# Performance work log

Measured on AMD Instinct MI355X. Metric: run time of the kernel, lower is better.

The kernel has to match this reference:

```python
import jax, jax.numpy as jnp
import numpy as np

N_NODES = 40000
N_EDGES = 640000
N_GRAPHS = 64
F_IN = 32       # fourier_order*4
D_EMB = 256     # int(0.5*512)
D_HID = 512     # int(0.5*1024)
D_FC = 1024     # int(0.5*2048)
N_CLS = 10


def setup_inputs() -> dict:
    key = jax.random.key(0)
    ks = iter(jax.random.split(key, 40))
    rn = lambda shape, s=0.05: jax.random.normal(next(ks), shape, jnp.float32) * s
    inp = {
        'x': jax.random.normal(next(ks), (N_NODES, F_IN), jnp.float32),
        'edge_index': jax.random.randint(next(ks), (2, N_EDGES), 0, N_NODES, jnp.int32),
        'edge_attr': jax.random.uniform(next(ks), (N_EDGES, 1), jnp.float32),
        'batch': jnp.sort(jax.random.randint(next(ks), (N_NODES,), 0, N_GRAPHS, jnp.int32)),
        # embedding MLP
        'emb_w1': rn((F_IN, D_EMB)), 'emb_b1': jnp.zeros((D_EMB,), jnp.float32),
        'emb_w2': rn((D_EMB, D_EMB)), 'emb_b2': jnp.zeros((D_EMB,), jnp.float32),
        # edge_proj MLP
        'ep_w1': rn((1, 64)), 'ep_b1': jnp.zeros((64,), jnp.float32),
        'ep_w2': rn((64, 1)), 'ep_b2': jnp.zeros((1,), jnp.float32),
        # GCNConv weights (x @ W + b, PyG convention)
        'w_c1': rn((D_EMB, D_HID)), 'b_c1': jnp.zeros((D_HID,), jnp.float32),
        'w_c2': rn((D_HID, D_HID)), 'b_c2': jnp.zeros((D_HID,), jnp.float32),
        'w_c3': rn((D_HID, D_HID)), 'b_c3': jnp.zeros((D_HID,), jnp.float32),
        'w_c4': rn((D_HID, D_HID)), 'b_c4': jnp.zeros((D_HID,), jnp.float32),
        'w_c5': rn((D_HID, D_HID)), 'b_c5': jnp.zeros((D_HID,), jnp.float32),
        'w_c6': rn((D_HID, D_HID)), 'b_c6': jnp.zeros((D_HID,), jnp.float32),
        # head
        'fc1_w': rn((D_HID, D_FC)), 'fc1_b': jnp.zeros((D_FC,), jnp.float32),
        'head_w': rn((D_FC, N_CLS)), 'head_b': jnp.zeros((N_CLS,), jnp.float32),
    }
    return inp


def _gcn_conv(x, src, dst, norm, W, b):
    # PyG GCNConv: linear transform, then normalized scatter-add aggregation, then bias
    h = x @ W                                   # [N, d_out]
    msg = h[src] * norm[:, None]                # [E+N, d_out] gathered messages
    agg = jax.ops.segment_sum(msg, dst, num_segments=N_NODES)
    return agg + b


def _forward(x, edge_attr, emb_w1, emb_b1, emb_w2, emb_b2, ep_w1, ep_b1, ep_w2, ep_b2,
             w_c1, b_c1, w_c2, b_c2, w_c3, b_c3, w_c4, b_c4, w_c5, b_c5, w_c6, b_c6,
             fc1_w, fc1_b, head_w, head_b, edge_index, batch):
    # edge weights from edge_proj MLP (sigmoid output in (0,1))
    ew = jax.nn.sigmoid(jax.nn.relu(edge_attr @ ep_w1 + ep_b1) @ ep_w2 + ep_b2)[:, 0]  # [E]
    # gcn_norm with self loops (identical for every conv layer -> compute once)
    loops = jnp.arange(N_NODES, dtype=edge_index.dtype)
    src = jnp.concatenate([edge_index[0], loops])
    dst = jnp.concatenate([edge_index[1], loops])
    w = jnp.concatenate([ew, jnp.ones((N_NODES,), ew.dtype)])
    deg = jax.ops.segment_sum(w, dst, num_segments=N_NODES)
    dinv = jnp.where(deg > 0, jax.lax.rsqrt(jnp.maximum(deg, 1e-12)), 0.0)
    norm = dinv[src] * w * dinv[dst]            # [E+N]

    h = jax.nn.relu(jax.nn.relu(x @ emb_w1 + emb_b1) @ emb_w2 + emb_b2)
    h = _gcn_conv(h, src, dst, norm, w_c1, b_c1)
    skip = jax.nn.relu(h)
    h = _gcn_conv(skip, src, dst, norm, w_c2, b_c2)
    h = jax.nn.relu(h)
    h = _gcn_conv(h, src, dst, norm, w_c3, b_c3)
    skip = jax.nn.relu(h) + skip                # has_skip=True
    h = _gcn_conv(skip, src, dst, norm, w_c4, b_c4)  # is_deep=True
    h = jax.nn.relu(h)
    h = _gcn_conv(h, src, dst, norm, w_c5, b_c5)
    h = jax.nn.relu(h)
    h = _gcn_conv(h, src, dst, norm, w_c6, b_c6)
    skip = jax.nn.relu(h) + skip

    # global mean pool over graphs
    sums = jax.ops.segment_sum(skip, batch, num_segments=N_GRAPHS)
    cnts = jax.ops.segment_sum(jnp.ones((N_NODES,), skip.dtype), batch, num_segments=N_GRAPHS)
    pooled = sums / jnp.maximum(cnts, 1.0)[:, None]   # [G, D_HID]

    out = jax.nn.relu(pooled @ fc1_w + fc1_b) @ head_w + head_b   # [G, N_CLS]
    return out


def reference(x, edge_index, edge_attr, batch, emb_w1, emb_b1, emb_w2, emb_b2,
              ep_w1, ep_b1, ep_w2, ep_b2, w_c1, b_c1, w_c2, b_c2, w_c3, b_c3,
              w_c4, b_c4, w_c5, b_c5, w_c6, b_c6, fc1_w, fc1_b, head_w, head_b):
    return _forward(x, edge_attr, emb_w1, emb_b1, emb_w2, emb_b2, ep_w1, ep_b1, ep_w2, ep_b2,
                    w_c1, b_c1, w_c2, b_c2, w_c3, b_c3, w_c4, b_c4, w_c5, b_c5, w_c6, b_c6,
                    fc1_w, fc1_b, head_w, head_b, edge_index, batch)
```

## Files before the change

kernel.cpp:

```cpp
#include <hip/hip_runtime.h>
#include <math.h>

#define N_NODES 40000
#define MP      40192
#define NROWB   157
#define N_EDGES 640000
#define N_GRAPHS 64
#define F_IN 32
#define D_EMB 256
#define D_HID 512
#define D_FC 1024
#define N_CLS 10

typedef _Float16 f16x8 __attribute__((ext_vector_type(8)));
typedef float f32x4  __attribute__((ext_vector_type(4)));
typedef unsigned short u16;

template <int N> struct VecU;
template <> struct VecU<2> { typedef unsigned T __attribute__((ext_vector_type(2))); };
template <> struct VecU<4> { typedef unsigned T __attribute__((ext_vector_type(4))); };

__device__ __forceinline__ float h2f(u16 u) {
    union { u16 s; _Float16 h; } v; v.s = u; return (float)v.h;
}
__device__ __forceinline__ u16 f2h(float f) {
    union { u16 s; _Float16 h; } v; v.h = (_Float16)f; return v.s;
}
__device__ __forceinline__ void async16(void* lds, const void* g) {
    __builtin_amdgcn_global_load_lds((const __attribute__((address_space(1))) void*)g,
                                     (__attribute__((address_space(3))) void*)lds, 16, 0, 0);
}

__global__ void edge_mlp_deg(const float* __restrict__ edge_attr,
                             const float* __restrict__ ep_w1, const float* __restrict__ ep_b1,
                             const float* __restrict__ ep_w2, const float* __restrict__ ep_b2,
                             const int* __restrict__ dst,
                             float* __restrict__ ew, float* __restrict__ deg, int* __restrict__ cnt) {
    __shared__ float w1[64], b1[64], w2[64];
    int t = threadIdx.x;
    if (t < 64) { w1[t] = ep_w1[t]; b1[t] = ep_b1[t]; w2[t] = ep_w2[t]; }
    __syncthreads();
    int e = blockIdx.x * blockDim.x + t;
    if (e >= N_EDGES) return;
    float x = edge_attr[e];
    float s = ep_b2[0];
#pragma unroll
    for (int j = 0; j < 64; ++j) s += fmaxf(x * w1[j] + b1[j], 0.f) * w2[j];
    float sig = 1.f / (1.f + expf(-s));
    ew[e] = sig;
    int d = dst[e];
    atomicAdd(&deg[d], sig);
    atomicAdd(&cnt[d], 1);
}

__global__ void init_kernel(float* __restrict__ deg, int* __restrict__ cnt, int* __restrict__ cursor) {
    int i = blockIdx.x * blockDim.x + threadIdx.x;
    if (i < N_NODES) { deg[i] = 1.0f; cnt[i] = 0; cursor[i] = 0; }
}

__global__ void dinv_kernel(const float* __restrict__ deg, float* __restrict__ dinv,
                            float* __restrict__ nloop) {
    int i = blockIdx.x * blockDim.x + threadIdx.x;
    if (i >= N_NODES) return;
    float d = deg[i];
    float r = (d > 0.f) ? rsqrtf(fmaxf(d, 1e-12f)) : 0.f;
    dinv[i] = r;
    nloop[i] = r * r;
}

__global__ void scan_kernel(const int* __restrict__ cnt, int* __restrict__ rowptr) {
    __shared__ int part[1024];
    int t = threadIdx.x;
    const int PER = (N_NODES + 1023) / 1024;
    int base = t * PER;
    int s = 0;
    for (int k = 0; k < PER; ++k) { int i = base + k; if (i < N_NODES) s += cnt[i]; }
    part[t] = s;
    __syncthreads();
    for (int off = 1; off < 1024; off <<= 1) {
        int v = (t >= off) ? part[t - off] : 0;
        __syncthreads();
        part[t] += v;
        __syncthreads();
    }
    int run = (t == 0) ? 0 : part[t - 1];
    for (int k = 0; k < PER; ++k) {
        int i = base + k;
        if (i < N_NODES) { rowptr[i] = run; run += cnt[i]; }
    }
    if (t == 1023) rowptr[N_NODES] = run;
}

__global__ void fill_csr_kernel(const int* __restrict__ src, const int* __restrict__ dst,
                                const float* __restrict__ ew, const float* __restrict__ dinv,
                                const int* __restrict__ rowptr, int* __restrict__ cursor,
                                int2* __restrict__ cv) {
    int e = blockIdx.x * blockDim.x + threadIdx.x;
    if (e >= N_EDGES) return;
    int d = dst[e];
    int s = src[e];
    float n = dinv[s] * ew[e] * dinv[d];
    int p = rowptr[d] + atomicAdd(&cursor[d], 1);
    cv[p] = make_int2(s, __float_as_int(n));
}

__global__ void wprep_kernel(const float* __restrict__ W, u16* __restrict__ Wt,
                             int K, int N) {
    __shared__ u16 th[32][33];
    int n0 = blockIdx.x * 32;
    int k0 = blockIdx.y * 32;
    int tx = threadIdx.x, ty = threadIdx.y;
#pragma unroll
    for (int r = 0; r < 4; ++r) {
        int k = ty + r * 8;
        th[k][tx] = f2h(W[(size_t)(k0 + k) * N + n0 + tx]);
    }
    __syncthreads();
#pragma unroll
    for (int r = 0; r < 4; ++r) {
        int n = ty + r * 8;
        Wt[(size_t)(n0 + n) * K + k0 + tx] = th[tx][n];
    }
}

__global__ void xprep_kernel(const float* __restrict__ x, u16* __restrict__ xb) {
    int idx = blockIdx.x * blockDim.x + threadIdx.x;
    if (idx >= MP * F_IN) return;
    int row = idx / F_IN;
    xb[idx] = (row < N_NODES) ? f2h(x[idx]) : (u16)0;
}

__global__ void gpad_zero(u16* __restrict__ G) {
    int i = blockIdx.x * blockDim.x + threadIdx.x;
    int total = (MP - N_NODES) * D_HID;
    if (i < total) G[(size_t)N_NODES * D_HID + i] = 0;
}

__launch_bounds__(512)
__global__ void mfma_gemm(const u16* __restrict__ A,
                          const u16* __restrict__ W,
                          const float* __restrict__ bias,
                          const u16* __restrict__ skip,
                          u16* __restrict__ C, int K, int N) {
    __shared__ __align__(16) u16 smem[2 * 12288];

    int nColB = N >> 7;
    int b = blockIdx.x;
    int rowI = (b >> 3) / nColB * 8 + (b & 7);
    int colI = (b >> 3) % nColB;
    if (rowI >= NROWB) return;
    int rowBase = rowI * 256;
    int colBase = colI * 128;

    int t = threadIdx.x;
    int lane = t & 63;
    int wave = t >> 6;
    int wr = wave >> 1;
    int wc = wave & 1;

    int tt  = (lane & 7) ^ ((lane >> 3) & 7);
    int rrl = ((lane >> 3) << 1) | (tt >> 2);
    int sel = (tt & 3) * 8;
    int r0A = wave * 32;
    int r0W = wave * 16;

    int quad = lane >> 4;
    int mrow = lane & 15;

    const u16* gA = A + (size_t)(rowBase + r0A + rrl) * K + sel;
    const u16* gW = W + (size_t)(colBase + r0W + rrl) * K + sel;

    f32x4 acc[4][4] = {};

    int nIter = K >> 5;
    {
        u16* As = smem; u16* Ws = smem + 8192;
        async16(&As[r0A * 32], gA);
        async16(&As[(r0A + 16) * 32], gA + (size_t)16 * K);
        async16(&Ws[r0W * 32], gW);
    }

    for (int it = 0; it < nIter; ++it) {
        int cur = it & 1;
        __syncthreads();
        if (it + 1 < nIter) {
            int k0 = (it + 1) << 5;
            u16* As = smem + (cur ^ 1) * 12288; u16* Ws = As + 8192;
            async16(&As[r0A * 32], gA + k0);
            async16(&As[(r0A + 16) * 32], gA + k0 + (size_t)16 * K);
            async16(&Ws[r0W * 32], gW + k0);
        }
        const u16* As = smem + cur * 12288;
        const u16* Ws = As + 8192;
        f16x8 af[4], wf[4];
#pragma unroll
        for (int i = 0; i < 4; ++i) {
            int Ra = wr * 64 + i * 16 + mrow;
            int sa = ((Ra & 1) * 4 + quad) ^ ((Ra >> 1) & 7);
            af[i] = *(const f16x8*)&As[(Ra >> 1) * 64 + sa * 8];
            int Rb = wc * 64 + i * 16 + mrow;
            int sb = ((Rb & 1) * 4 + quad) ^ ((Rb >> 1) & 7);
            wf[i] = *(const f16x8*)&Ws[(Rb >> 1) * 64 + sb * 8];
        }
#pragma unroll
        for (int i = 0; i < 4; ++i)
#pragma unroll
            for (int j = 0; j < 4; ++j)
                acc[i][j] = __builtin_amdgcn_mfma_f32_16x16x32_f16(af[i], wf[j], acc[i][j], 0, 0, 0);
    }
    __syncthreads();

    const int ES = 132;
    u16* eb = smem;
#pragma unroll
    for (int ph = 0; ph < 2; ++ph) {
        if ((wr >> 1) == ph) {
#pragma unroll
            for (int j = 0; j < 4; ++j) {
                int col = colBase + wc * 64 + j * 16 + mrow;
                float bv = bias[col];
#pragma unroll
                for (int i = 0; i < 4; ++i) {
#pragma unroll
                    for (int r = 0; r < 4; ++r) {
                        int lr = (wr & 1) * 64 + i * 16 + quad * 4 + r;
                        size_t row = (size_t)rowBase + ph * 128 + lr;
                        float v = fmaxf(acc[i][j][r] + bv, 0.f);
                        if (skip) v += h2f(skip[row * N + col]);
                        eb[lr * ES + wc * 64 + j * 16 + mrow] = f2h(v);
                    }
                }
            }
        }
        __syncthreads();
#pragma unroll
        for (int k = 0; k < 4; ++k) {
            int c = t + k * 512;
            int row = c >> 4;
            int ch = c & 15;
            f16x8 v = *(const f16x8*)&eb[row * ES + ch * 8];
            *(f16x8*)&C[(size_t)(rowBase + ph * 128 + row) * N + colBase + ch * 8] = v;
        }
        __syncthreads();
    }
}

template <int D>
__launch_bounds__(256)
__global__ void gather_f16(const u16* __restrict__ h, const int* __restrict__ rowptr,
                           const int2* __restrict__ cv, const float* __restrict__ nloop,
                           u16* __restrict__ out) {
    constexpr int FPL = D / 64;
    constexpr int UPL = FPL / 2;
    using VU = typename VecU<UPL>::T;
    int node = blockIdx.x * 4 + (threadIdx.x >> 6);
    int lane = threadIdx.x & 63;
    if (node >= N_NODES) return;
    union UU { unsigned u; _Float16 h[2]; };
    float acc[FPL];
    float sl = nloop[node];
    {
        VU own = *(const VU*)(h + (size_t)node * D + lane * FPL);
#pragma unroll
        for (int u = 0; u < UPL; ++u) {
            UU w; w.u = own[u];
            acc[2 * u]     = (float)w.h[0] * sl;
            acc[2 * u + 1] = (float)w.h[1] * sl;
        }
    }
    int beg = rowptr[node], end = rowptr[node + 1];
    if (end > beg) {
        int last = end - 1;
        int2 c[8];
#pragma unroll
        for (int m = 0; m < 8; ++m) c[m] = cv[min(beg + m, last)];
        for (int j = beg; j < end; j += 8) {
            VU tv[8];
#pragma unroll
            for (int m = 0; m < 8; ++m)
                tv[m] = *(const VU*)(h + (size_t)c[m].x * D + lane * FPL);
            int jn = j + 8;
            int2 cn[8];
#pragma unroll
            for (int m = 0; m < 8; ++m) cn[m] = c[m];
            if (jn < end) {
#pragma unroll
                for (int m = 0; m < 8; ++m) cn[m] = cv[min(jn + m, last)];
            }
            __builtin_amdgcn_sched_barrier(0);
#pragma unroll
            for (int m = 0; m < 8; ++m) {
                float v = (j + m < end) ? __int_as_float(c[m].y) : 0.f;
#pragma unroll
                for (int u = 0; u < UPL; ++u) {
                    UU w; w.u = tv[m][u];
                    acc[2 * u]     += (float)w.h[0] * v;
                    acc[2 * u + 1] += (float)w.h[1] * v;
                }
            }
#pragma unroll
            for (int m = 0; m < 8; ++m) c[m] = cn[m];
        }
    }
    VU o;
#pragma unroll
    for (int u = 0; u < UPL; ++u) {
        unsigned lo = f2h(acc[2 * u]);
        unsigned hi = f2h(acc[2 * u + 1]);
        o[u] = lo | (hi << 16);
    }
    *(VU*)(out + (size_t)node * D + lane * FPL) = o;
}

#define NP 50
__global__ void pool_sum_f16(const u16* __restrict__ x, const int* __restrict__ batch,
                             float* __restrict__ sums) {
    int t = blockIdx.x * blockDim.x + threadIdx.x;
    int total = (N_NODES / NP) * D_HID;
    if (t >= total) return;
    int d = t % D_HID;
    int group = t / D_HID;
    int n0 = group * NP;
    float acc = 0.f;
    int g = batch[n0];
    for (int k = 0; k < NP; ++k) {
        int n = n0 + k;
        int bg = batch[n];
        if (bg != g) { atomicAdd(&sums[(size_t)g * D_HID + d], acc); acc = 0.f; g = bg; }
        acc += h2f(x[(size_t)n * D_HID + d]);
    }
    atomicAdd(&sums[(size_t)g * D_HID + d], acc);
}

__global__ void graph_cnt_kernel(const int* __restrict__ batch, float* __restrict__ cnts) {
    int g = threadIdx.x;
    if (g >= N_GRAPHS) return;
    int lo = 0, hi = N_NODES;
    while (lo < hi) { int m = (lo + hi) >> 1; if (batch[m] < g) lo = m + 1; else hi = m; }
    int lb = lo;
    lo = lb; hi = N_NODES;
    while (lo < hi) { int m = (lo + hi) >> 1; if (batch[m] < g + 1) lo = m + 1; else hi = m; }
    cnts[g] = (float)(lo - lb);
}

__global__ void zero2_kernel(float* __restrict__ p1, int n1, float* __restrict__ p2, int n2) {
    int i = blockIdx.x * blockDim.x + threadIdx.x;
    if (i < n1) p1[i] = 0.f;
    else if (i < n1 + n2) p2[i - n1] = 0.f;
}

__launch_bounds__(256)
__global__ void fc1_part(const float* __restrict__ sums, const float* __restrict__ cnts,
                         const float* __restrict__ fc1_w, float* __restrict__ F) {
    __shared__ float sv[64];
    int b = blockIdx.x;
    int g = b >> 3;
    int kc = b & 7;
    int t = threadIdx.x;
    if (t < 64) sv[t] = sums[(size_t)g * D_HID + kc * 64 + t] / fmaxf(cnts[g], 1.f);
    __syncthreads();
#pragma unroll
    for (int m = 0; m < D_FC / 256; ++m) {
        int j = t + m * 256;
        const float* wp = fc1_w + (size_t)(kc * 64) * D_FC + j;
        float acc = 0.f;
#pragma unroll
        for (int k = 0; k < 64; ++k) acc += sv[k] * wp[(size_t)k * D_FC];
        atomicAdd(&F[(size_t)g * D_FC + j], acc);
    }
}

__launch_bounds__(256)
__global__ void head_final(const float* __restrict__ F, const float* __restrict__ fc1_b,
                           const float* __restrict__ head_w, const float* __restrict__ head_b,
                           float* __restrict__ out) {
    __shared__ float hacc[N_CLS];
    int g = blockIdx.x;
    int t = threadIdx.x;
    if (t < N_CLS) hacc[t] = 0.f;
    __syncthreads();
    float p[N_CLS] = {};
    for (int j = t; j < D_FC; j += 256) {
        float f = fmaxf(F[(size_t)g * D_FC + j] + fc1_b[j], 0.f);
#pragma unroll
        for (int c = 0; c < N_CLS; ++c) p[c] += f * head_w[j * N_CLS + c];
    }
#pragma unroll
    for (int c = 0; c < N_CLS; ++c) {
        float v = p[c];
        for (int off = 32; off; off >>= 1) v += __shfl_down(v, off, 64);
        if ((t & 63) == 0) atomicAdd(&hacc[c], v);
    }
    __syncthreads();
    if (t < N_CLS) out[g * N_CLS + t] = hacc[t] + head_b[t];
}

extern "C" void kernel_launch(void* const* d_in, const int* in_sizes, int n_in,
                              void* d_out, int out_size, void* d_ws, size_t ws_size,
                              hipStream_t stream) {
    const float* x          = (const float*)d_in[0];
    const int*   edge_index = (const int*)d_in[1];
    const float* edge_attr  = (const float*)d_in[2];
    const int*   batch      = (const int*)d_in[3];
    const float* emb_w1 = (const float*)d_in[4];
    const float* emb_b1 = (const float*)d_in[5];
    const float* emb_w2 = (const float*)d_in[6];
    const float* emb_b2 = (const float*)d_in[7];
    const float* ep_w1  = (const float*)d_in[8];
    const float* ep_b1  = (const float*)d_in[9];
    const float* ep_w2  = (const float*)d_in[10];
    const float* ep_b2  = (const float*)d_in[11];
    const float* w_c[6] = { (const float*)d_in[12], (const float*)d_in[14], (const float*)d_in[16],
                            (const float*)d_in[18], (const float*)d_in[20], (const float*)d_in[22] };
    const float* b_c[6] = { (const float*)d_in[13], (const float*)d_in[15], (const float*)d_in[17],
                            (const float*)d_in[19], (const float*)d_in[21], (const float*)d_in[23] };
    const float* fc1_w  = (const float*)d_in[24];
    const float* fc1_b  = (const float*)d_in[25];
    const float* head_w = (const float*)d_in[26];
    const float* head_b = (const float*)d_in[27];
    float* out = (float*)d_out;

    const int* src = edge_index;
    const int* dst = edge_index + N_EDGES;

    char* p = (char*)d_ws;
    auto alloc = [&](size_t bytes) { char* r = p; p += (bytes + 255) & ~(size_t)255; return r; };
    float* ew    = (float*)alloc(N_EDGES * 4);
    float* deg   = (float*)alloc(N_NODES * 4);
    float* dinv  = (float*)alloc(N_NODES * 4);
    float* nloop = (float*)alloc(N_NODES * 4);
    int* cnt     = (int*)alloc(N_NODES * 4);
    int* cursor  = (int*)alloc(N_NODES * 4);
    int* rowptr  = (int*)alloc((N_NODES + 1) * 4);
    int2* cv     = (int2*)alloc((size_t)N_EDGES * 8);
    u16* xb = (u16*)alloc((size_t)MP * F_IN * 2);
    u16* H1 = (u16*)alloc((size_t)MP * D_EMB * 2);
    u16* H2 = (u16*)alloc((size_t)MP * D_EMB * 2);
    u16* G  = (u16*)alloc((size_t)MP * D_HID * 2);
    u16* S1 = (u16*)alloc((size_t)MP * D_HID * 2);
    u16* S2 = (u16*)alloc((size_t)MP * D_HID * 2);
    u16* Cb = (u16*)alloc((size_t)MP * D_HID * 2);
    u16* we1 = (u16*)alloc((size_t)F_IN * D_EMB * 2);
    u16* we2 = (u16*)alloc((size_t)D_EMB * D_EMB * 2);
    u16* wc[6];
    wc[0] = (u16*)alloc((size_t)D_EMB * D_HID * 2);
    for (int i = 1; i < 6; ++i) wc[i] = (u16*)alloc((size_t)D_HID * D_HID * 2);
    float* sums = (float*)alloc(N_GRAPHS * D_HID * 4);
    float* cnts = (float*)alloc(N_GRAPHS * 4);
    float* F    = (float*)alloc(N_GRAPHS * D_FC * 4);

    const int TB = 256;
    const int EB = (N_EDGES + TB - 1) / TB;
    const int NB = (N_NODES + TB - 1) / TB;

    init_kernel<<<NB, TB, 0, stream>>>(deg, cnt, cursor);
    edge_mlp_deg<<<EB, TB, 0, stream>>>(edge_attr, ep_w1, ep_b1, ep_w2, ep_b2, dst, ew, deg, cnt);
    dinv_kernel<<<NB, TB, 0, stream>>>(deg, dinv, nloop);
    scan_kernel<<<1, 1024, 0, stream>>>(cnt, rowptr);
    fill_csr_kernel<<<EB, TB, 0, stream>>>(src, dst, ew, dinv, rowptr, cursor, cv);

    xprep_kernel<<<(MP * F_IN + TB - 1) / TB, TB, 0, stream>>>(x, xb);
    gpad_zero<<<((MP - N_NODES) * D_HID + TB - 1) / TB, TB, 0, stream>>>(G);
    wprep_kernel<<<dim3(D_EMB / 32, F_IN / 32), dim3(32, 8), 0, stream>>>(emb_w1, we1, F_IN, D_EMB);
    wprep_kernel<<<dim3(D_EMB / 32, D_EMB / 32), dim3(32, 8), 0, stream>>>(emb_w2, we2, D_EMB, D_EMB);
    wprep_kernel<<<dim3(D_HID / 32, D_EMB / 32), dim3(32, 8), 0, stream>>>(w_c[0], wc[0], D_EMB, D_HID);
    for (int i = 1; i < 6; ++i)
        wprep_kernel<<<dim3(D_HID / 32, D_HID / 32), dim3(32, 8), 0, stream>>>(w_c[i], wc[i], D_HID, D_HID);

    const int SLOTS = ((NROWB + 7) / 8) * 8;
    const int GRID2 = SLOTS * (D_EMB / 128);
    const int GRID4 = SLOTS * (D_HID / 128);
    mfma_gemm<<<GRID2, 512, 0, stream>>>(xb, we1, emb_b1, nullptr, H1, F_IN, D_EMB);
    mfma_gemm<<<GRID2, 512, 0, stream>>>(H1, we2, emb_b2, nullptr, H2, D_EMB, D_EMB);

    const int GG = (N_NODES + 3) / 4;
    gather_f16<D_EMB><<<GG, 256, 0, stream>>>(H2, rowptr, cv, nloop, G);
    mfma_gemm<<<GRID4, 512, 0, stream>>>(G, wc[0], b_c[0], nullptr, S1, D_EMB, D_HID);
    gather_f16<D_HID><<<GG, 256, 0, stream>>>(S1, rowptr, cv, nloop, G);
    mfma_gemm<<<GRID4, 512, 0, stream>>>(G, wc[1], b_c[1], nullptr, Cb, D_HID, D_HID);
    gather_f16<D_HID><<<GG, 256, 0, stream>>>(Cb, rowptr, cv, nloop, G);
    mfma_gemm<<<GRID4, 512, 0, stream>>>(G, wc[2], b_c[2], S1, S2, D_HID, D_HID);
    gather_f16<D_HID><<<GG, 256, 0, stream>>>(S2, rowptr, cv, nloop, G);
    mfma_gemm<<<GRID4, 512, 0, stream>>>(G, wc[3], b_c[3], nullptr, Cb, D_HID, D_HID);
    gather_f16<D_HID><<<GG, 256, 0, stream>>>(Cb, rowptr, cv, nloop, G);
    mfma_gemm<<<GRID4, 512, 0, stream>>>(G, wc[4], b_c[4], nullptr, Cb, D_HID, D_HID);
    gather_f16<D_HID><<<GG, 256, 0, stream>>>(Cb, rowptr, cv, nloop, G);
    mfma_gemm<<<GRID4, 512, 0, stream>>>(G, wc[5], b_c[5], S2, Cb, D_HID, D_HID);

    zero2_kernel<<<(N_GRAPHS * (D_HID + D_FC) + TB - 1) / TB, TB, 0, stream>>>(
        sums, N_GRAPHS * D_HID, F, N_GRAPHS * D_FC);
    pool_sum_f16<<<((N_NODES / NP) * D_HID + TB - 1) / TB, TB, 0, stream>>>(Cb, batch, sums);
    graph_cnt_kernel<<<1, 64, 0, stream>>>(batch, cnts);
    fc1_part<<<N_GRAPHS * 8, 256, 0, stream>>>(sums, cnts, fc1_w, F);
    head_final<<<N_GRAPHS, 256, 0, stream>>>(F, fc1_b, head_w, head_b, out);
}
```

Measured before the change: 1.197 ms.

## Fuse prep kernels, batch weight transposes, fuse mean-pool into last GEMM epilogue

Merges the init, x-conversion, pad-zero and sums-zero kernels into one launch, and folds the eight weight transposes into a single grid indexed by blockIdx.z. The last GCN GEMM now accumulates the global sum pool straight from its LDS epilogue tile with atomics and no longer writes its output. The fc1 and head kernels become one per-graph kernel that also computes node counts. This cuts launch count and one full activation write and read, at the cost of a serial per-block fc1 loop. Output stores are also switched to nontemporal.

```diff
diff --git a/kernel.cpp b/kernel.cpp
--- a/kernel.cpp
+++ b/kernel.cpp
@@ -31,6 +31,19 @@
                                      (__attribute__((address_space(3))) void*)lds, 16, 0, 0);
 }
 
+__global__ void prep_all(const float* __restrict__ x, u16* __restrict__ xb, u16* __restrict__ G,
+                         float* __restrict__ deg, int* __restrict__ cnt, int* __restrict__ cursor,
+                         float* __restrict__ sums) {
+    int i = blockIdx.x * blockDim.x + threadIdx.x;
+    if (i < N_NODES) { deg[i] = 1.0f; cnt[i] = 0; cursor[i] = 0; }
+    if (i < MP * F_IN) {
+        int row = i >> 5;
+        xb[i] = (row < N_NODES) ? f2h(x[i]) : (u16)0;
+    }
+    if (i < (MP - N_NODES) * D_HID) G[(size_t)N_NODES * D_HID + i] = 0;
+    if (i < N_GRAPHS * D_HID) sums[i] = 0.f;
+}
+
 __global__ void edge_mlp_deg(const float* __restrict__ edge_attr,
                              const float* __restrict__ ep_w1, const float* __restrict__ ep_b1,
                              const float* __restrict__ ep_w2, const float* __restrict__ ep_b2,
@@ -51,11 +64,6 @@
     int d = dst[e];
     atomicAdd(&deg[d], sig);
     atomicAdd(&cnt[d], 1);
-}
-
-__global__ void init_kernel(float* __restrict__ deg, int* __restrict__ cnt, int* __restrict__ cursor) {
-    int i = blockIdx.x * blockDim.x + threadIdx.x;
-    if (i < N_NODES) { deg[i] = 1.0f; cnt[i] = 0; cursor[i] = 0; }
 }
 
 __global__ void dinv_kernel(const float* __restrict__ deg, float* __restrict__ dinv,
@@ -104,36 +112,27 @@
     cv[p] = make_int2(s, __float_as_int(n));
 }
 
-__global__ void wprep_kernel(const float* __restrict__ W, u16* __restrict__ Wt,
-                             int K, int N) {
+struct WPair { const float* s; u16* d; int K; int N; };
+struct WP8 { WPair m[8]; };
+
+__global__ void wprep_all(WP8 a) {
     __shared__ u16 th[32][33];
+    WPair w = a.m[blockIdx.z];
     int n0 = blockIdx.x * 32;
     int k0 = blockIdx.y * 32;
+    if (n0 >= w.N || k0 >= w.K) return;
     int tx = threadIdx.x, ty = threadIdx.y;
 #pragma unroll
     for (int r = 0; r < 4; ++r) {
         int k = ty + r * 8;
-        th[k][tx] = f2h(W[(size_t)(k0 + k) * N + n0 + tx]);
+        th[k][tx] = f2h(w.s[(size_t)(k0 + k) * w.N + n0 + tx]);
     }
     __syncthreads();
 #pragma unroll
     for (int r = 0; r < 4; ++r) {
         int n = ty + r * 8;
-        Wt[(size_t)(n0 + n) * K + k0 + tx] = th[tx][n];
-    }
-}
-
-__global__ void xprep_kernel(const float* __restrict__ x, u16* __restrict__ xb) {
-    int idx = blockIdx.x * blockDim.x + threadIdx.x;
-    if (idx >= MP * F_IN) return;
-    int row = idx / F_IN;
-    xb[idx] = (row < N_NODES) ? f2h(x[idx]) : (u16)0;
-}
-
-__global__ void gpad_zero(u16* __restrict__ G) {
-    int i = blockIdx.x * blockDim.x + threadIdx.x;
-    int total = (MP - N_NODES) * D_HID;
-    if (i < total) G[(size_t)N_NODES * D_HID + i] = 0;
+        w.d[(size_t)(n0 + n) * w.K + k0 + tx] = th[tx][n];
+    }
 }
 
 __launch_bounds__(512)
@@ -141,8 +140,10 @@
                           const u16* __restrict__ W,
                           const float* __restrict__ bias,
                           const u16* __restrict__ skip,
-                          u16* __restrict__ C, int K, int N) {
+                          u16* __restrict__ C, int K, int N,
+                          const int* __restrict__ batch, float* __restrict__ pool) {
     __shared__ __align__(16) u16 smem[2 * 12288];
+    __shared__ int sbatch[128];
 
     int nColB = N >> 7;
     int b = blockIdx.x;
@@ -232,14 +233,35 @@
                 }
             }
         }
+        if (pool && t < 128) {
+            int row = rowBase + ph * 128 + t;
+            sbatch[t] = (row < N_NODES) ? batch[row] : -1;
+        }
         __syncthreads();
-#pragma unroll
-        for (int k = 0; k < 4; ++k) {
-            int c = t + k * 512;
-            int row = c >> 4;
-            int ch = c & 15;
-            f16x8 v = *(const f16x8*)&eb[row * ES + ch * 8];
-            *(f16x8*)&C[(size_t)(rowBase + ph * 128 + row) * N + colBase + ch * 8] = v;
+        if (C) {
+#pragma unroll
+            for (int k = 0; k < 4; ++k) {
+                int c = t + k * 512;
+                int row = c >> 4;
+                int ch = c & 15;
+                f16x8 v = *(const f16x8*)&eb[row * ES + ch * 8];
+                __builtin_nontemporal_store(v,
+                    (f16x8*)&C[(size_t)(rowBase + ph * 128 + row) * N + colBase + ch * 8]);
+            }
+        }
+        if (pool) {
+            int c = t & 127;
+            int rs = (t >> 7) * 32;
+            float run = 0.f; int g = -1;
+            for (int r = rs; r < rs + 32; ++r) {
+                int bg = sbatch[r];
+                if (bg != g) {
+                    if (g >= 0) atomicAdd(&pool[(size_t)g * D_HID + colBase + c], run);
+                    run = 0.f; g = bg;
+                }
+                if (bg >= 0) run += h2f(eb[r * ES + c]);
+            }
+            if (g >= 0) atomicAdd(&pool[(size_t)g * D_HID + colBase + c], run);
         }
         __syncthreads();
     }
@@ -309,79 +331,43 @@
         unsigned hi = f2h(acc[2 * u + 1]);
         o[u] = lo | (hi << 16);
     }
-    *(VU*)(out + (size_t)node * D + lane * FPL) = o;
-}
-
-#define NP 50
-__global__ void pool_sum_f16(const u16* __restrict__ x, const int* __restrict__ batch,
-                             float* __restrict__ sums) {
-    int t = blockIdx.x * blockDim.x + threadIdx.x;
-    int total = (N_NODES / NP) * D_HID;
-    if (t >= total) return;
-    int d = t % D_HID;
-    int group = t / D_HID;
-    int n0 = group * NP;
-    float acc = 0.f;
-    int g = batch[n0];
-    for (int k = 0; k < NP; ++k) {
-        int n = n0 + k;
-        int bg = batch[n];
-        if (bg != g) { atomicAdd(&sums[(size_t)g * D_HID + d], acc); acc = 0.f; g = bg; }
-        acc += h2f(x[(size_t)n * D_HID + d]);
-    }
-    atomicAdd(&sums[(size_t)g * D_HID + d], acc);
-}
-
-__global__ void graph_cnt_kernel(const int* __restrict__ batch, float* __restrict__ cnts) {
-    int g = threadIdx.x;
-    if (g >= N_GRAPHS) return;
-    int lo = 0, hi = N_NODES;
-    while (lo < hi) { int m = (lo + hi) >> 1; if (batch[m] < g) lo = m + 1; else hi = m; }
-    int lb = lo;
-    lo = lb; hi = N_NODES;
-    while (lo < hi) { int m = (lo + hi) >> 1; if (batch[m] < g + 1) lo = m + 1; else hi = m; }
-    cnts[g] = (float)(lo - lb);
-}
-
-__global__ void zero2_kernel(float* __restrict__ p1, int n1, float* __restrict__ p2, int n2) {
-    int i = blockIdx.x * blockDim.x + threadIdx.x;
-    if (i < n1) p1[i] = 0.f;
-    else if (i < n1 + n2) p2[i - n1] = 0.f;
+    __builtin_nontemporal_store(o, (VU*)(out + (size_t)node * D + lane * FPL));
 }
 
 __launch_bounds__(256)
-__global__ void fc1_part(const float* __restrict__ sums, const float* __restrict__ cnts,
-                         const float* __restrict__ fc1_w, float* __restrict__ F) {
-    __shared__ float sv[64];
-    int b = blockIdx.x;
-    int g = b >> 3;
-    int kc = b & 7;
+__global__ void fc1_head(const float* __restrict__ sums, const int* __restrict__ batch,
+                         const float* __restrict__ fc1_w, const float* __restrict__ fc1_b,
+                         const float* __restrict__ head_w, const float* __restrict__ head_b,
+                         float* __restrict__ out) {
+    __shared__ float sv[D_HID];
+    __shared__ float fj[D_FC];
+    __shared__ float hacc[N_CLS];
+    __shared__ float invc;
+    int g = blockIdx.x;
     int t = threadIdx.x;
-    if (t < 64) sv[t] = sums[(size_t)g * D_HID + kc * 64 + t] / fmaxf(cnts[g], 1.f);
+    if (t == 0) {
+        int lo = 0, hi = N_NODES;
+        while (lo < hi) { int m = (lo + hi) >> 1; if (batch[m] < g) lo = m + 1; else hi = m; }
+        int lb = lo;
+        lo = lb; hi = N_NODES;
+        while (lo < hi) { int m = (lo + hi) >> 1; if (batch[m] < g + 1) lo = m + 1; else hi = m; }
+        invc = 1.f / fmaxf((float)(lo - lb), 1.f);
+    }
+    if (t < N_CLS) hacc[t] = 0.f;
+    __syncthreads();
+    for (int k = t; k < D_HID; k += 256) sv[k] = sums[(size_t)g * D_HID + k] * invc;
     __syncthreads();
 #pragma unroll
     for (int m = 0; m < D_FC / 256; ++m) {
         int j = t + m * 256;
-        const float* wp = fc1_w + (size_t)(kc * 64) * D_FC + j;
-        float acc = 0.f;
-#pragma unroll
-        for (int k = 0; k < 64; ++k) acc += sv[k] * wp[(size_t)k * D_FC];
-        atomicAdd(&F[(size_t)g * D_FC + j], acc);
-    }
-}
-
-__launch_bounds__(256)
-__global__ void head_final(const float* __restrict__ F, const float* __restrict__ fc1_b,
-                           const float* __restrict__ head_w, const float* __restrict__ head_b,
-                           float* __restrict__ out) {
-    __shared__ float hacc[N_CLS];
-    int g = blockIdx.x;
-    int t = threadIdx.x;
-    if (t < N_CLS) hacc[t] = 0.f;
+        float acc = fc1_b[j];
+        for (int k = 0; k < D_HID; ++k) acc += sv[k] * fc1_w[(size_t)k * D_FC + j];
+        fj[j] = fmaxf(acc, 0.f);
+    }
     __syncthreads();
     float p[N_CLS] = {};
     for (int j = t; j < D_FC; j += 256) {
-        float f = fmaxf(F[(size_t)g * D_FC + j] + fc1_b[j], 0.f);
+        float f = fj[j];
 #pragma unroll
         for (int c = 0; c < N_CLS; ++c) p[c] += f * head_w[j * N_CLS + c];
     }
@@ -446,51 +432,43 @@
     wc[0] = (u16*)alloc((size_t)D_EMB * D_HID * 2);
     for (int i = 1; i < 6; ++i) wc[i] = (u16*)alloc((size_t)D_HID * D_HID * 2);
     float* sums = (float*)alloc(N_GRAPHS * D_HID * 4);
-    float* cnts = (float*)alloc(N_GRAPHS * 4);
-    float* F    = (float*)alloc(N_GRAPHS * D_FC * 4);
 
     const int TB = 256;
     const int EB = (N_EDGES + TB - 1) / TB;
     const int NB = (N_NODES + TB - 1) / TB;
 
-    init_kernel<<<NB, TB, 0, stream>>>(deg, cnt, cursor);
+    prep_all<<<(MP * F_IN + TB - 1) / TB, TB, 0, stream>>>(x, xb, G, deg, cnt, cursor, sums);
     edge_mlp_deg<<<EB, TB, 0, stream>>>(edge_attr, ep_w1, ep_b1, ep_w2, ep_b2, dst, ew, deg, cnt);
     dinv_kernel<<<NB, TB, 0, stream>>>(deg, dinv, nloop);
     scan_kernel<<<1, 1024, 0, stream>>>(cnt, rowptr);
     fill_csr_kernel<<<EB, TB, 0, stream>>>(src, dst, ew, dinv, rowptr, cursor, cv);
 
-    xprep_kernel<<<(MP * F_IN + TB - 1) / TB, TB, 0, stream>>>(x, xb);
-    gpad_zero<<<((MP - N_NODES) * D_HID + TB - 1) / TB, TB, 0, stream>>>(G);
-    wprep_kernel<<<dim3(D_EMB / 32, F_IN / 32), dim3(32, 8), 0, stream>>>(emb_w1, we1, F_IN, D_EMB);
-    wprep_kernel<<<dim3(D_EMB / 32, D_EMB / 32), dim3(32, 8), 0, stream>>>(emb_w2, we2, D_EMB, D_EMB);
-    wprep_kernel<<<dim3(D_HID / 32, D_EMB / 32), dim3(32, 8), 0, stream>>>(w_c[0], wc[0], D_EMB, D_HID);
-    for (int i = 1; i < 6; ++i)
-        wprep_kernel<<<dim3(D_HID / 32, D_HID / 32), dim3(32, 8), 0, stream>>>(w_c[i], wc[i], D_HID, D_HID);
+    WP8 wp;
+    wp.m[0] = { emb_w1, we1, F_IN,  D_EMB };
+    wp.m[1] = { emb_w2, we2, D_EMB, D_EMB };
+    wp.m[2] = { w_c[0], wc[0], D_EMB, D_HID };
+    for (int i = 1; i < 6; ++i) wp.m[2 + i] = { w_c[i], wc[i], D_HID, D_HID };
+    wprep_all<<<dim3(16, 16, 8), dim3(32, 8), 0, stream>>>(wp);
 
     const int SLOTS = ((NROWB + 7) / 8) * 8;
     const int GRID2 = SLOTS * (D_EMB / 128);
     const int GRID4 = SLOTS * (D_HID / 128);
-    mfma_gemm<<<GRID2, 512, 0, stream>>>(xb, we1, emb_b1, nullptr, H1, F_IN, D_EMB);
-    mfma_gemm<<<GRID2, 512, 0, stream>>>(H1, we2, emb_b2, nullptr, H2, D_EMB, D_EMB);
+    mfma_gemm<<<GRID2, 512, 0, stream>>>(xb, we1, emb_b1, nullptr, H1, F_IN, D_EMB, nullptr, nullptr);
+    mfma_gemm<<<GRID2, 512, 0, stream>>>(H1, we2, emb_b2, nullptr, H2, D_EMB, D_EMB, nullptr, nullptr);
 
     const int GG = (N_NODES + 3) / 4;
     gather_f16<D_EMB><<<GG, 256, 0, stream>>>(H2, rowptr, cv, nloop, G);
-    mfma_gemm<<<GRID4, 512, 0, stream>>>(G, wc[0], b_c[0], nullptr, S1, D_EMB, D_HID);
+    mfma_gemm<<<GRID4, 512, 0, stream>>>(G, wc[0], b_c[0], nullptr, S1, D_EMB, D_HID, nullptr, nullptr);
     gather_f16<D_HID><<<GG, 256, 0, stream>>>(S1, rowptr, cv, nloop, G);
-    mfma_gemm<<<GRID4, 512, 0, stream>>>(G, wc[1], b_c[1], nullptr, Cb, D_HID, D_HID);
+    mfma_gemm<<<GRID4, 512, 0, stream>>>(G, wc[1], b_c[1], nullptr, Cb, D_HID, D_HID, nullptr, nullptr);
     gather_f16<D_HID><<<GG, 256, 0, stream>>>(Cb, rowptr, cv, nloop, G);
-    mfma_gemm<<<GRID4, 512, 0, stream>>>(G, wc[2], b_c[2], S1, S2, D_HID, D_HID);
+    mfma_gemm<<<GRID4, 512, 0, stream>>>(G, wc[2], b_c[2], S1, S2, D_HID, D_HID, nullptr, nullptr);
     gather_f16<D_HID><<<GG, 256, 0, stream>>>(S2, rowptr, cv, nloop, G);
-    mfma_gemm<<<GRID4, 512, 0, stream>>>(G, wc[3], b_c[3], nullptr, Cb, D_HID, D_HID);
+    mfma_gemm<<<GRID4, 512, 0, stream>>>(G, wc[3], b_c[3], nullptr, Cb, D_HID, D_HID, nullptr, nullptr);
     gather_f16<D_HID><<<GG, 256, 0, stream>>>(Cb, rowptr, cv, nloop, G);
-    mfma_gemm<<<GRID4, 512, 0, stream>>>(G, wc[4], b_c[4], nullptr, Cb, D_HID, D_HID);
+    mfma_gemm<<<GRID4, 512, 0, stream>>>(G, wc[4], b_c[4], nullptr, Cb, D_HID, D_HID, nullptr, nullptr);
     gather_f16<D_HID><<<GG, 256, 0, stream>>>(Cb, rowptr, cv, nloop, G);
-    mfma_gemm<<<GRID4, 512, 0, stream>>>(G, wc[5], b_c[5], S2, Cb, D_HID, D_HID);
-
-    zero2_kernel<<<(N_GRAPHS * (D_HID + D_FC) + TB - 1) / TB, TB, 0, stream>>>(
-        sums, N_GRAPHS * D_HID, F, N_GRAPHS * D_FC);
-    pool_sum_f16<<<((N_NODES / NP) * D_HID + TB - 1) / TB, TB, 0, stream>>>(Cb, batch, sums);
-    graph_cnt_kernel<<<1, 64, 0, stream>>>(batch, cnts);
-    fc1_part<<<N_GRAPHS * 8, 256, 0, stream>>>(sums, cnts, fc1_w, F);
-    head_final<<<N_GRAPHS, 256, 0, stream>>>(F, fc1_b, head_w, head_b, out);
-}
+    mfma_gemm<<<GRID4, 512, 0, stream>>>(G, wc[5], b_c[5], S2, nullptr, D_HID, D_HID, batch, sums);
+
+    fc1_head<<<N_GRAPHS, 256, 0, stream>>>(sums, batch, fc1_w, fc1_b, head_w, head_b, out);
+}
```

Result: slower. 1.266 ms (+5.8%).
